# Kernel optimization log

Measured on AMD Instinct MI355X. Metric: run time of the kernel, lower is better.

Reference implementation:

```python
import jax, jax.numpy as jnp
import numpy as np

N, D, K = 40000, 64, 16
E = N * K
EPS = 1e-5  # torch BatchNorm1d default eps


def _bn(h, g, b):
    # BatchNorm1d in training mode: biased batch statistics over dim 0
    m = h.mean(0)
    v = h.var(0)
    return (h - m) * jax.lax.rsqrt(v + EPS) * g + b


def setup_inputs() -> dict:
    key = jax.random.key(0)
    ks = jax.random.split(key, 4)
    kp = jax.random.split(ks[3], 9)

    def w(k, shape):
        return (jax.random.normal(k, shape, dtype=jnp.float32) / np.float32(np.sqrt(shape[0])))

    src = jax.random.randint(ks[2], (E,), 0, N, dtype=jnp.int32)
    dst = jnp.repeat(jnp.arange(N, dtype=jnp.int32), K)  # kNN-style: each node has K in-edges

    return {
        "x": jax.random.normal(ks[0], (N, D), dtype=jnp.float32),
        "pos": jax.random.normal(ks[1], (N, 3), dtype=jnp.float32),
        "edge_index": jnp.stack([src, dst]),
        "W_in": w(kp[0], (D, D)),
        "g1": jnp.ones(D), "b1": jnp.zeros(D),
        "W_v": w(kp[1], (D, D)),
        "W_src": w(kp[2], (D, D)),
        "W_dst": w(kp[3], (D, D)),
        "Wp1": w(kp[4], (3, 3)), "bp1": jnp.zeros(3),
        "gp": jnp.ones(3), "bp": jnp.zeros(3),
        "Wp2": w(kp[5], (3, D)), "bp2": jnp.zeros(D),
        "ga0": jnp.ones(D), "ba0": jnp.zeros(D),
        "Wa1": w(kp[6], (D, D // 8)), "ba1": jnp.zeros(D // 8),
        "ga1": jnp.ones(D // 8), "bb1": jnp.zeros(D // 8),
        "Wa2": w(kp[7], (D // 8, D)), "ba2": jnp.zeros(D),
        "g2": jnp.ones(D), "b2": jnp.zeros(D),
        "W_out": w(kp[8], (D, D)),
        "g3": jnp.ones(D), "b3": jnp.zeros(D),
    }


def reference(x, pos, edge_index, W_in, g1, b1, W_v, W_src, W_dst,
              Wp1, bp1, gp, bp, Wp2, bp2, ga0, ba0, Wa1, ba1, ga1, bb1,
              Wa2, ba2, g2, b2, W_out, g3, b3):
    src, dst = edge_index[0], edge_index[1]  # j (source), i (dest)
    n = x.shape[0]
    x_skip = x
    h = jax.nn.relu(_bn(x @ W_in, g1, b1))

    # PointTransformerConv
    a_src = h @ W_src            # alpha_j projection [N,D]
    a_dst = h @ W_dst            # alpha_i projection [N,D]
    v = h @ W_v                  # value projection  [N,D]
    rel = pos[dst] - pos[src]    # pos_i - pos_j     [E,3]
    ph = jax.nn.relu(_bn(rel @ Wp1 + bp1, gp, bp))
    delta = ph @ Wp2 + bp2       # pos_nn output     [E,D]
    a = a_dst[dst] - a_src[src] + delta
    # attn_nn: BN -> ReLU -> (Lin+BN+ReLU) -> Lin
    a = jax.nn.relu(_bn(a, ga0, ba0))
    a = jax.nn.relu(_bn(a @ Wa1 + ba1, ga1, bb1))
    a = a @ Wa2 + ba2            # [E,D]
    # segment-wise softmax over incoming edges of each dest node
    amax = jax.lax.stop_gradient(jax.ops.segment_max(a, dst, num_segments=n))
    e = jnp.exp(a - amax[dst])
    s = jax.ops.segment_sum(e, dst, num_segments=n)
    attn = e / (s[dst] + 1e-16)  # PyG softmax adds 1e-16
    agg = jax.ops.segment_sum(attn * (v[src] + delta), dst, num_segments=n)

    h = jax.nn.relu(_bn(agg, g2, b2))
    h = _bn(h @ W_out, g3, b3)
    return jax.nn.relu(h + x_skip)
```

## Files before the change

### kernel.cpp

```cpp
#include <hip/hip_runtime.h>

#define NN 40000
#define DDIM 64
#define KE 16
#define EE 640000
#define BNEPS 1e-5f

__device__ __forceinline__ void bn_coeff(const float* __restrict__ S, int C, int c,
                                         const float* __restrict__ g, const float* __restrict__ b,
                                         float inv_n, float& sc, float& sh)
{
    float m   = S[c] * inv_n;
    float var = S[C + c] * inv_n - m * m;
    float r   = rsqrtf(var + BNEPS);
    sc = g[c] * r;
    sh = b[c] - m * sc;
}

template<int TRN>
__global__ __launch_bounds__(256) void gemm64_k(
    const float* __restrict__ in,
    const float* __restrict__ W0, const float* __restrict__ W1, const float* __restrict__ W2,
    float* __restrict__ out0, float* __restrict__ out1, float* __restrict__ out2,
    const float* __restrict__ Sin, const float* __restrict__ gamma, const float* __restrict__ beta,
    float inv_n, float* __restrict__ Sout)
{
    const float* W = (blockIdx.y == 0) ? W0 : ((blockIdx.y == 1) ? W1 : W2);
    float* out     = (blockIdx.y == 0) ? out0 : ((blockIdx.y == 1) ? out1 : out2);

    __shared__ float Wl[64][64];
    __shared__ float inl[64][65];
    __shared__ float scl[64], shl[64];
    __shared__ float ssum[64], ssq[64];

    const int t = threadIdx.x;
    if (t < 64) {
        if (TRN) { float sc, sh; bn_coeff(Sin, 64, t, gamma, beta, inv_n, sc, sh); scl[t] = sc; shl[t] = sh; }
        ssum[t] = 0.f; ssq[t] = 0.f;
    }
#pragma unroll
    for (int i = 0; i < 16; i++) { int idx = t + i * 256; Wl[idx >> 6][idx & 63] = W[idx]; }
    __syncthreads();

    const int rbase = blockIdx.x * 64;
    {
        const int d = t & 63;
        float sc = 0.f, sh = 0.f;
        if (TRN) { sc = scl[d]; sh = shl[d]; }
#pragma unroll
        for (int i = 0; i < 16; i++) {
            int r = (t >> 6) + i * 4;
            float v = in[(size_t)(rbase + r) * 64 + d];
            if (TRN) v = fmaxf(fmaf(v, sc, sh), 0.f);
            inl[r][d] = v;
        }
    }
    __syncthreads();

    const int c0 = (t & 15) * 4, r0 = (t >> 4) * 4;
    float acc[4][4] = {};
#pragma unroll 16
    for (int d = 0; d < 64; d++) {
        float4 w4 = *(const float4*)&Wl[d][c0];
#pragma unroll
        for (int i = 0; i < 4; i++) {
            float h = inl[r0 + i][d];
            acc[i][0] = fmaf(h, w4.x, acc[i][0]);
            acc[i][1] = fmaf(h, w4.y, acc[i][1]);
            acc[i][2] = fmaf(h, w4.z, acc[i][2]);
            acc[i][3] = fmaf(h, w4.w, acc[i][3]);
        }
    }
#pragma unroll
    for (int i = 0; i < 4; i++) {
        float4 o; o.x = acc[i][0]; o.y = acc[i][1]; o.z = acc[i][2]; o.w = acc[i][3];
        *(float4*)&out[(size_t)(rbase + r0 + i) * 64 + c0] = o;
    }
    if (Sout) {
#pragma unroll
        for (int j = 0; j < 4; j++) {
            float s  = acc[0][j] + acc[1][j] + acc[2][j] + acc[3][j];
            float qv = acc[0][j] * acc[0][j] + acc[1][j] * acc[1][j] + acc[2][j] * acc[2][j] + acc[3][j] * acc[3][j];
            atomicAdd(&ssum[c0 + j], s);
            atomicAdd(&ssq[c0 + j], qv);
        }
        __syncthreads();
        if (t < 64) { atomicAdd(&Sout[t], ssum[t]); atomicAdd(&Sout[64 + t], ssq[t]); }
    }
}

__global__ __launch_bounds__(256) void edge_q_k(
    const float* __restrict__ pos, const int* __restrict__ src,
    const float* __restrict__ Wp1, const float* __restrict__ bp1,
    float* __restrict__ q0, float* __restrict__ q1, float* __restrict__ q2,
    float* __restrict__ Sq)
{
    float w00 = Wp1[0], w01 = Wp1[1], w02 = Wp1[2];
    float w10 = Wp1[3], w11 = Wp1[4], w12 = Wp1[5];
    float w20 = Wp1[6], w21 = Wp1[7], w22 = Wp1[8];
    float c0 = bp1[0], c1 = bp1[1], c2 = bp1[2];
    float s0 = 0, s1 = 0, s2 = 0, p0 = 0, p1 = 0, p2 = 0;
    for (int e = blockIdx.x * blockDim.x + threadIdx.x; e < EE; e += gridDim.x * blockDim.x) {
        int sj = src[e]; int di = e >> 4;
        float r0 = pos[di * 3 + 0] - pos[sj * 3 + 0];
        float r1 = pos[di * 3 + 1] - pos[sj * 3 + 1];
        float r2 = pos[di * 3 + 2] - pos[sj * 3 + 2];
        float v0 = c0 + r0 * w00 + r1 * w10 + r2 * w20;
        float v1 = c1 + r0 * w01 + r1 * w11 + r2 * w21;
        float v2 = c2 + r0 * w02 + r1 * w12 + r2 * w22;
        q0[e] = v0; q1[e] = v1; q2[e] = v2;
        s0 += v0; s1 += v1; s2 += v2;
        p0 += v0 * v0; p1 += v1 * v1; p2 += v2 * v2;
    }
#pragma unroll
    for (int o = 32; o > 0; o >>= 1) {
        s0 += __shfl_down(s0, o); s1 += __shfl_down(s1, o); s2 += __shfl_down(s2, o);
        p0 += __shfl_down(p0, o); p1 += __shfl_down(p1, o); p2 += __shfl_down(p2, o);
    }
    __shared__ float sred[4][6];
    const int w = threadIdx.x >> 6;
    if ((threadIdx.x & 63) == 0) {
        sred[w][0] = s0; sred[w][1] = s1; sred[w][2] = s2;
        sred[w][3] = p0; sred[w][4] = p1; sred[w][5] = p2;
    }
    __syncthreads();
    if (threadIdx.x < 6) {
        float v = sred[0][threadIdx.x] + sred[1][threadIdx.x] + sred[2][threadIdx.x] + sred[3][threadIdx.x];
        atomicAdd(&Sq[threadIdx.x], v);
    }
}

__global__ __launch_bounds__(256) void edge_a0_k(
    const float* __restrict__ q0, const float* __restrict__ q1, const float* __restrict__ q2,
    const int* __restrict__ src,
    const float* __restrict__ adst, const float* __restrict__ asrc,
    const float* __restrict__ Wp2, const float* __restrict__ bp2,
    const float* __restrict__ Sq, const float* __restrict__ gp, const float* __restrict__ bp_,
    float* __restrict__ Sa0)
{
    const int lane = threadIdx.x & 63;
    const int r = lane >> 4, fq = lane & 15;
    const int wv   = blockIdx.x * (blockDim.x >> 6) + (threadIdx.x >> 6);
    const int nwv  = gridDim.x * (blockDim.x >> 6);
    const float inv_e = 1.0f / (float)EE;
    float sc30, sh30, sc31, sh31, sc32, sh32;
    bn_coeff(Sq, 3, 0, gp, bp_, inv_e, sc30, sh30);
    bn_coeff(Sq, 3, 1, gp, bp_, inv_e, sc31, sh31);
    bn_coeff(Sq, 3, 2, gp, bp_, inv_e, sc32, sh32);
    float4 w0_4 = *(const float4*)&Wp2[fq * 4];
    float4 w1_4 = *(const float4*)&Wp2[64 + fq * 4];
    float4 w2_4 = *(const float4*)&Wp2[128 + fq * 4];
    float4 bd4  = *(const float4*)&bp2[fq * 4];
    float4 s4 = {0.f,0.f,0.f,0.f}, p4 = {0.f,0.f,0.f,0.f};

    for (int i = wv; i < NN; i += nwv) {
        const int e0 = i << 4;
        float4 ad4 = *(const float4*)&adst[(size_t)i * 64 + fq * 4];
        int   sv  = src[e0 + (lane & 15)];
        float qv0 = q0[e0 + (lane & 15)];
        float qv1 = q1[e0 + (lane & 15)];
        float qv2 = q2[e0 + (lane & 15)];
        int sj[4];
#pragma unroll
        for (int p = 0; p < 4; p++) sj[p] = __shfl(sv, p * 4 + r);
        float4 av[4];
#pragma unroll
        for (int p = 0; p < 4; p++) av[p] = *(const float4*)&asrc[(size_t)sj[p] * 64 + fq * 4];
#pragma unroll
        for (int p = 0; p < 4; p++) {
            int j = p * 4 + r;
            float ph0 = fmaxf(fmaf(__shfl(qv0, j), sc30, sh30), 0.f);
            float ph1 = fmaxf(fmaf(__shfl(qv1, j), sc31, sh31), 0.f);
            float ph2 = fmaxf(fmaf(__shfl(qv2, j), sc32, sh32), 0.f);
            float4 a0v;
            a0v.x = ad4.x - av[p].x + bd4.x + ph0 * w0_4.x + ph1 * w1_4.x + ph2 * w2_4.x;
            a0v.y = ad4.y - av[p].y + bd4.y + ph0 * w0_4.y + ph1 * w1_4.y + ph2 * w2_4.y;
            a0v.z = ad4.z - av[p].z + bd4.z + ph0 * w0_4.z + ph1 * w1_4.z + ph2 * w2_4.z;
            a0v.w = ad4.w - av[p].w + bd4.w + ph0 * w0_4.w + ph1 * w1_4.w + ph2 * w2_4.w;
            s4.x += a0v.x; s4.y += a0v.y; s4.z += a0v.z; s4.w += a0v.w;
            p4.x = fmaf(a0v.x, a0v.x, p4.x); p4.y = fmaf(a0v.y, a0v.y, p4.y);
            p4.z = fmaf(a0v.z, a0v.z, p4.z); p4.w = fmaf(a0v.w, a0v.w, p4.w);
        }
    }
    s4.x += __shfl_xor(s4.x, 16); s4.y += __shfl_xor(s4.y, 16);
    s4.z += __shfl_xor(s4.z, 16); s4.w += __shfl_xor(s4.w, 16);
    p4.x += __shfl_xor(p4.x, 16); p4.y += __shfl_xor(p4.y, 16);
    p4.z += __shfl_xor(p4.z, 16); p4.w += __shfl_xor(p4.w, 16);
    s4.x += __shfl_xor(s4.x, 32); s4.y += __shfl_xor(s4.y, 32);
    s4.z += __shfl_xor(s4.z, 32); s4.w += __shfl_xor(s4.w, 32);
    p4.x += __shfl_xor(p4.x, 32); p4.y += __shfl_xor(p4.y, 32);
    p4.z += __shfl_xor(p4.z, 32); p4.w += __shfl_xor(p4.w, 32);

    __shared__ float ls[64], lq[64];
    if (threadIdx.x < 64) { ls[threadIdx.x] = 0.f; lq[threadIdx.x] = 0.f; }
    __syncthreads();
    if (lane < 16) {
        atomicAdd(&ls[fq * 4 + 0], s4.x); atomicAdd(&ls[fq * 4 + 1], s4.y);
        atomicAdd(&ls[fq * 4 + 2], s4.z); atomicAdd(&ls[fq * 4 + 3], s4.w);
        atomicAdd(&lq[fq * 4 + 0], p4.x); atomicAdd(&lq[fq * 4 + 1], p4.y);
        atomicAdd(&lq[fq * 4 + 2], p4.z); atomicAdd(&lq[fq * 4 + 3], p4.w);
    }
    __syncthreads();
    if (threadIdx.x < 64) { atomicAdd(&Sa0[threadIdx.x], ls[threadIdx.x]); atomicAdd(&Sa0[64 + threadIdx.x], lq[threadIdx.x]); }
}

__global__ __launch_bounds__(256) void edge_t_k(
    const float* __restrict__ q0, const float* __restrict__ q1, const float* __restrict__ q2,
    const int* __restrict__ src,
    const float* __restrict__ adst, const float* __restrict__ asrc,
    const float* __restrict__ Wp2, const float* __restrict__ bp2,
    const float* __restrict__ Sq, const float* __restrict__ gp, const float* __restrict__ bp_,
    const float* __restrict__ Sa0, const float* __restrict__ ga0, const float* __restrict__ ba0,
    const float* __restrict__ Wa1, const float* __restrict__ ba1,
    float* __restrict__ tout, float* __restrict__ St)
{
    __shared__ float a1l[64][68];
    __shared__ float wl[64][8];
    __shared__ float red[16];
    const int t = threadIdx.x;
    const int lane = t & 63;
    const int w = t >> 6;
    const int r = lane >> 4, fq = lane & 15;
    const float inv_e = 1.0f / (float)EE;
    float sc30, sh30, sc31, sh31, sc32, sh32;
    bn_coeff(Sq, 3, 0, gp, bp_, inv_e, sc30, sh30);
    bn_coeff(Sq, 3, 1, gp, bp_, inv_e, sc31, sh31);
    bn_coeff(Sq, 3, 2, gp, bp_, inv_e, sc32, sh32);
    float4 scA4, shA4;
    bn_coeff(Sa0, 64, fq * 4 + 0, ga0, ba0, inv_e, scA4.x, shA4.x);
    bn_coeff(Sa0, 64, fq * 4 + 1, ga0, ba0, inv_e, scA4.y, shA4.y);
    bn_coeff(Sa0, 64, fq * 4 + 2, ga0, ba0, inv_e, scA4.z, shA4.z);
    bn_coeff(Sa0, 64, fq * 4 + 3, ga0, ba0, inv_e, scA4.w, shA4.w);
    float4 w0_4 = *(const float4*)&Wp2[fq * 4];
    float4 w1_4 = *(const float4*)&Wp2[64 + fq * 4];
    float4 w2_4 = *(const float4*)&Wp2[128 + fq * 4];
    float4 bd4  = *(const float4*)&bp2[fq * 4];
    for (int i = t; i < 512; i += 256) wl[i >> 3][i & 7] = Wa1[i];
    if (t < 16) red[t] = 0.f;

    const int eL = t >> 2;
    const int j0 = (t & 3) * 2;
    float bA = ba1[j0], bB = ba1[j0 + 1];
    float ssA = 0.f, spA = 0.f, ssB = 0.f, spB = 0.f;

    for (int g = blockIdx.x; g < NN / 4; g += gridDim.x) {
        __syncthreads();
        {
            const int i  = g * 4 + w;
            const int e0 = i << 4;
            float4 ad4 = *(const float4*)&adst[(size_t)i * 64 + fq * 4];
            int   sv  = src[e0 + (lane & 15)];
            float qv0 = q0[e0 + (lane & 15)];
            float qv1 = q1[e0 + (lane & 15)];
            float qv2 = q2[e0 + (lane & 15)];
            int sj[4];
#pragma unroll
            for (int p = 0; p < 4; p++) sj[p] = __shfl(sv, p * 4 + r);
            float4 av[4];
#pragma unroll
            for (int p = 0; p < 4; p++) av[p] = *(const float4*)&asrc[(size_t)sj[p] * 64 + fq * 4];
#pragma unroll
            for (int p = 0; p < 4; p++) {
                int j = p * 4 + r;
                float ph0 = fmaxf(fmaf(__shfl(qv0, j), sc30, sh30), 0.f);
                float ph1 = fmaxf(fmaf(__shfl(qv1, j), sc31, sh31), 0.f);
                float ph2 = fmaxf(fmaf(__shfl(qv2, j), sc32, sh32), 0.f);
                float4 a1v;
                a1v.x = ad4.x - av[p].x + bd4.x + ph0 * w0_4.x + ph1 * w1_4.x + ph2 * w2_4.x;
                a1v.y = ad4.y - av[p].y + bd4.y + ph0 * w0_4.y + ph1 * w1_4.y + ph2 * w2_4.y;
                a1v.z = ad4.z - av[p].z + bd4.z + ph0 * w0_4.z + ph1 * w1_4.z + ph2 * w2_4.z;
                a1v.w = ad4.w - av[p].w + bd4.w + ph0 * w0_4.w + ph1 * w1_4.w + ph2 * w2_4.w;
                a1v.x = fmaxf(fmaf(a1v.x, scA4.x, shA4.x), 0.f);
                a1v.y = fmaxf(fmaf(a1v.y, scA4.y, shA4.y), 0.f);
                a1v.z = fmaxf(fmaf(a1v.z, scA4.z, shA4.z), 0.f);
                a1v.w = fmaxf(fmaf(a1v.w, scA4.w, shA4.w), 0.f);
                *(float4*)&a1l[w * 16 + j][fq * 4] = a1v;
            }
        }
        __syncthreads();
        {
            float acc0 = bA, acc1 = bB;
#pragma unroll 16
            for (int dd = 0; dd < 64; dd++) {
                float a = a1l[eL][dd];
                acc0 = fmaf(a, wl[dd][j0], acc0);
                acc1 = fmaf(a, wl[dd][j0 + 1], acc1);
            }
            int e = g * 64 + eL;
            float2 o; o.x = acc0; o.y = acc1;
            *(float2*)&tout[(size_t)e * 8 + j0] = o;
            ssA += acc0; spA += acc0 * acc0;
            ssB += acc1; spB += acc1 * acc1;
        }
    }
    __syncthreads();
    atomicAdd(&red[j0], ssA);     atomicAdd(&red[j0 + 1], ssB);
    atomicAdd(&red[8 + j0], spA); atomicAdd(&red[8 + j0 + 1], spB);
    __syncthreads();
    if (t < 16) atomicAdd(&St[t], red[t]);
}

__global__ __launch_bounds__(256) void edge_final_k(
    const float* __restrict__ tin,
    const float* __restrict__ q0, const float* __restrict__ q1, const float* __restrict__ q2,
    const int* __restrict__ src, const float* __restrict__ vv,
    const float* __restrict__ Wp2, const float* __restrict__ bp2,
    const float* __restrict__ Sq, const float* __restrict__ gp, const float* __restrict__ bp_,
    const float* __restrict__ St, const float* __restrict__ ga1, const float* __restrict__ bb1,
    const float* __restrict__ Wa2, const float* __restrict__ ba2,
    float* __restrict__ agg, float* __restrict__ Sagg)
{
    __shared__ float att_l[4][16][68];
    __shared__ float tt_l[4][16][8];
    __shared__ float ls[64], lq[64];
    const int t = threadIdx.x, lane = t & 63, w = t >> 6;
    const int r = lane >> 4, fq = lane & 15;
    const float inv_e = 1.0f / (float)EE;
    float sc3[3], sh3[3];
#pragma unroll
    for (int k = 0; k < 3; k++) bn_coeff(Sq, 3, k, gp, bp_, inv_e, sc3[k], sh3[k]);
    float sc8[8], sh8[8];
#pragma unroll
    for (int k = 0; k < 8; k++) bn_coeff(St, 8, k, ga1, bb1, inv_e, sc8[k], sh8[k]);
    float wa[8];
#pragma unroll
    for (int k = 0; k < 8; k++) wa[k] = Wa2[k * 64 + lane];
    float bad = ba2[lane];
    float4 wp0_4 = *(const float4*)&Wp2[fq * 4];
    float4 wp1_4 = *(const float4*)&Wp2[64 + fq * 4];
    float4 wp2_4 = *(const float4*)&Wp2[128 + fq * 4];
    float4 bpd4  = *(const float4*)&bp2[fq * 4];
    float4 ssum4 = {0.f, 0.f, 0.f, 0.f}, ssq4 = {0.f, 0.f, 0.f, 0.f};

    for (int nn = 0; nn < 4; nn++) {
        const int i  = blockIdx.x * 16 + nn * 4 + w;
        const int e0 = i << 4;
        if (lane < 32) {
            float4 v = *(const float4*)&tin[(size_t)e0 * 8 + lane * 4];
            ((float4*)&tt_l[w][0][0])[lane] = v;
        }
        int   sv  = src[e0 + (lane & 15)];
        float qv0 = q0[e0 + (lane & 15)];
        float qv1 = q1[e0 + (lane & 15)];
        float qv2 = q2[e0 + (lane & 15)];
        __syncthreads();
        {
            float ax[16];
            float m = -3.0e38f;
#pragma unroll
            for (int j = 0; j < 16; j++) {
                float4 ta = *(const float4*)&tt_l[w][j][0];
                float4 tb = *(const float4*)&tt_l[w][j][4];
                float a = bad;
                a = fmaf(fmaxf(fmaf(ta.x, sc8[0], sh8[0]), 0.f), wa[0], a);
                a = fmaf(fmaxf(fmaf(ta.y, sc8[1], sh8[1]), 0.f), wa[1], a);
                a = fmaf(fmaxf(fmaf(ta.z, sc8[2], sh8[2]), 0.f), wa[2], a);
                a = fmaf(fmaxf(fmaf(ta.w, sc8[3], sh8[3]), 0.f), wa[3], a);
                a = fmaf(fmaxf(fmaf(tb.x, sc8[4], sh8[4]), 0.f), wa[4], a);
                a = fmaf(fmaxf(fmaf(tb.y, sc8[5], sh8[5]), 0.f), wa[5], a);
                a = fmaf(fmaxf(fmaf(tb.z, sc8[6], sh8[6]), 0.f), wa[6], a);
                a = fmaf(fmaxf(fmaf(tb.w, sc8[7], sh8[7]), 0.f), wa[7], a);
                ax[j] = a; m = fmaxf(m, a);
            }
            float s = 0.f;
#pragma unroll
            for (int j = 0; j < 16; j++) { ax[j] = __expf(ax[j] - m); s += ax[j]; }
            float inv = 1.0f / (s + 1e-16f);
#pragma unroll
            for (int j = 0; j < 16; j++) att_l[w][j][lane] = ax[j] * inv;
        }
        __syncthreads();
        {
            float4 acc = {0.f, 0.f, 0.f, 0.f};
#pragma unroll
            for (int p = 0; p < 4; p++) {
                int j  = p * 4 + r;
                int sj = __shfl(sv, j);
                float4 v4  = *(const float4*)&vv[(size_t)sj * 64 + fq * 4];
                float4 at4 = *(const float4*)&att_l[w][j][fq * 4];
                float ph0 = fmaxf(fmaf(__shfl(qv0, j), sc3[0], sh3[0]), 0.f);
                float ph1 = fmaxf(fmaf(__shfl(qv1, j), sc3[1], sh3[1]), 0.f);
                float ph2 = fmaxf(fmaf(__shfl(qv2, j), sc3[2], sh3[2]), 0.f);
                float4 dl4;
                dl4.x = bpd4.x + ph0 * wp0_4.x + ph1 * wp1_4.x + ph2 * wp2_4.x;
                dl4.y = bpd4.y + ph0 * wp0_4.y + ph1 * wp1_4.y + ph2 * wp2_4.y;
                dl4.z = bpd4.z + ph0 * wp0_4.z + ph1 * wp1_4.z + ph2 * wp2_4.z;
                dl4.w = bpd4.w + ph0 * wp0_4.w + ph1 * wp1_4.w + ph2 * wp2_4.w;
                acc.x = fmaf(at4.x, v4.x + dl4.x, acc.x);
                acc.y = fmaf(at4.y, v4.y + dl4.y, acc.y);
                acc.z = fmaf(at4.z, v4.z + dl4.z, acc.z);
                acc.w = fmaf(at4.w, v4.w + dl4.w, acc.w);
            }
            acc.x += __shfl_xor(acc.x, 16); acc.y += __shfl_xor(acc.y, 16);
            acc.z += __shfl_xor(acc.z, 16); acc.w += __shfl_xor(acc.w, 16);
            acc.x += __shfl_xor(acc.x, 32); acc.y += __shfl_xor(acc.y, 32);
            acc.z += __shfl_xor(acc.z, 32); acc.w += __shfl_xor(acc.w, 32);
            if (lane < 16) {
                *(float4*)&agg[(size_t)i * 64 + lane * 4] = acc;
                ssum4.x += acc.x; ssum4.y += acc.y; ssum4.z += acc.z; ssum4.w += acc.w;
                ssq4.x  += acc.x * acc.x; ssq4.y += acc.y * acc.y;
                ssq4.z  += acc.z * acc.z; ssq4.w += acc.w * acc.w;
            }
        }
        __syncthreads();
    }
    if (t < 64) { ls[t] = 0.f; lq[t] = 0.f; }
    __syncthreads();
    if (lane < 16) {
        atomicAdd(&ls[fq * 4 + 0], ssum4.x); atomicAdd(&ls[fq * 4 + 1], ssum4.y);
        atomicAdd(&ls[fq * 4 + 2], ssum4.z); atomicAdd(&ls[fq * 4 + 3], ssum4.w);
        atomicAdd(&lq[fq * 4 + 0], ssq4.x);  atomicAdd(&lq[fq * 4 + 1], ssq4.y);
        atomicAdd(&lq[fq * 4 + 2], ssq4.z);  atomicAdd(&lq[fq * 4 + 3], ssq4.w);
    }
    __syncthreads();
    if (t < 64) { atomicAdd(&Sagg[t], ls[t]); atomicAdd(&Sagg[64 + t], lq[t]); }
}

__global__ __launch_bounds__(256) void final_k(
    const float* __restrict__ t2, const float* __restrict__ x,
    const float* __restrict__ St2, const float* __restrict__ g3, const float* __restrict__ b3,
    float* __restrict__ out)
{
    __shared__ float scl[64], shl[64];
    const int t = threadIdx.x;
    if (t < 64) { float sc, sh; bn_coeff(St2, 64, t, g3, b3, 1.0f / (float)NN, sc, sh); scl[t] = sc; shl[t] = sh; }
    __syncthreads();
    int idx = blockIdx.x * 256 + t;
    int c0 = (idx & 15) * 4;
    const float4 a = *(const float4*)&t2[(size_t)idx * 4];
    const float4 b = *(const float4*)&x[(size_t)idx * 4];
    float4 o;
    o.x = fmaxf(fmaf(a.x, scl[c0 + 0], shl[c0 + 0]) + b.x, 0.f);
    o.y = fmaxf(fmaf(a.y, scl[c0 + 1], shl[c0 + 1]) + b.y, 0.f);
    o.z = fmaxf(fmaf(a.z, scl[c0 + 2], shl[c0 + 2]) + b.z, 0.f);
    o.w = fmaxf(fmaf(a.w, scl[c0 + 3], shl[c0 + 3]) + b.w, 0.f);
    *(float4*)&out[(size_t)idx * 4] = o;
}

extern "C" void kernel_launch(void* const* d_in, const int* in_sizes, int n_in,
                              void* d_out, int out_size, void* d_ws, size_t ws_size,
                              hipStream_t stream)
{
    const float* x    = (const float*)d_in[0];
    const float* pos  = (const float*)d_in[1];
    const int*   src  = (const int*)d_in[2];
    const float* W_in = (const float*)d_in[3];
    const float* g1   = (const float*)d_in[4];
    const float* b1   = (const float*)d_in[5];
    const float* W_v  = (const float*)d_in[6];
    const float* W_src= (const float*)d_in[7];
    const float* W_dst= (const float*)d_in[8];
    const float* Wp1  = (const float*)d_in[9];
    const float* bp1  = (const float*)d_in[10];
    const float* gp   = (const float*)d_in[11];
    const float* bp_  = (const float*)d_in[12];
    const float* Wp2  = (const float*)d_in[13];
    const float* bp2  = (const float*)d_in[14];
    const float* ga0  = (const float*)d_in[15];
    const float* ba0  = (const float*)d_in[16];
    const float* Wa1  = (const float*)d_in[17];
    const float* ba1  = (const float*)d_in[18];
    const float* ga1  = (const float*)d_in[19];
    const float* bb1  = (const float*)d_in[20];
    const float* Wa2  = (const float*)d_in[21];
    const float* ba2  = (const float*)d_in[22];
    const float* g2   = (const float*)d_in[23];
    const float* b2   = (const float*)d_in[24];
    const float* W_out= (const float*)d_in[25];
    const float* g3   = (const float*)d_in[26];
    const float* b3   = (const float*)d_in[27];
    float* out = (float*)d_out;

    float* wsf   = (float*)d_ws;
    float* S_t1  = wsf;
    float* S_q   = wsf + 128;
    float* S_a0  = wsf + 192;
    float* S_t   = wsf + 320;
    float* S_agg = wsf + 384;
    float* S_t2  = wsf + 512;
    const size_t N64 = (size_t)NN * 64;
    float* t1   = wsf + 1024;
    float* asrc = t1 + N64;
    float* adst = asrc + N64;
    float* vv   = adst + N64;
    float* q0   = vv + N64;
    float* q1   = q0 + EE;
    float* q2   = q1 + EE;
    float* tt   = q2 + EE;
    float* agg  = t1;
    float* t2   = asrc;

    hipMemsetAsync(wsf, 0, 1024 * sizeof(float), stream);

    gemm64_k<0><<<dim3(625, 1), 256, 0, stream>>>(x, W_in, W_in, W_in, t1, t1, t1,
                                                  nullptr, nullptr, nullptr, 0.f, S_t1);
    gemm64_k<1><<<dim3(625, 3), 256, 0, stream>>>(t1, W_src, W_dst, W_v, asrc, adst, vv,
                                                  S_t1, g1, b1, 1.0f / (float)NN, nullptr);
    edge_q_k<<<256, 256, 0, stream>>>(pos, src, Wp1, bp1, q0, q1, q2, S_q);
    edge_a0_k<<<2048, 256, 0, stream>>>(q0, q1, q2, src, adst, asrc, Wp2, bp2, S_q, gp, bp_, S_a0);
    edge_t_k<<<2048, 256, 0, stream>>>(q0, q1, q2, src, adst, asrc, Wp2, bp2, S_q, gp, bp_,
                                       S_a0, ga0, ba0, Wa1, ba1, tt, S_t);
    edge_final_k<<<2500, 256, 0, stream>>>(tt, q0, q1, q2, src, vv, Wp2, bp2, S_q, gp, bp_,
                                           S_t, ga1, bb1, Wa2, ba2, agg, S_agg);
    gemm64_k<1><<<dim3(625, 1), 256, 0, stream>>>(agg, W_out, W_out, W_out, t2, t2, t2,
                                                  S_agg, g2, b2, 1.0f / (float)NN, S_t2);
    final_k<<<2500, 256, 0, stream>>>(t2, x, S_t2, g3, b3, out);
}
```

Before: 292.7 us.

## Pack per-edge q and src into float4; compute Wa1 projection in registers with shuffles

Per-edge position features q0/q1/q2 and the source index are now stored together as one float4 per edge. The three edge kernels fetch them with a single vector load instead of four scalar loads. edge_t_k drops its shared-memory staging of the activations and its two block barriers per group. Each lane now multiplies its 4 features by a register-held slice of Wa1 and the 8 outputs are summed across 16 lanes with xor shuffles. This adds many shuffles and more register use per edge in exchange for less shared-memory traffic and synchronisation.

```diff
diff --git a/kernel.cpp b/kernel.cpp
--- a/kernel.cpp
+++ b/kernel.cpp
@@ -92,8 +92,7 @@
 __global__ __launch_bounds__(256) void edge_q_k(
     const float* __restrict__ pos, const int* __restrict__ src,
     const float* __restrict__ Wp1, const float* __restrict__ bp1,
-    float* __restrict__ q0, float* __restrict__ q1, float* __restrict__ q2,
-    float* __restrict__ Sq)
+    float4* __restrict__ q4, float* __restrict__ Sq)
 {
     float w00 = Wp1[0], w01 = Wp1[1], w02 = Wp1[2];
     float w10 = Wp1[3], w11 = Wp1[4], w12 = Wp1[5];
@@ -108,7 +107,8 @@
         float v0 = c0 + r0 * w00 + r1 * w10 + r2 * w20;
         float v1 = c1 + r0 * w01 + r1 * w11 + r2 * w21;
         float v2 = c2 + r0 * w02 + r1 * w12 + r2 * w22;
-        q0[e] = v0; q1[e] = v1; q2[e] = v2;
+        float4 o; o.x = v0; o.y = v1; o.z = v2; o.w = __int_as_float(sj);
+        q4[e] = o;
         s0 += v0; s1 += v1; s2 += v2;
         p0 += v0 * v0; p1 += v1 * v1; p2 += v2 * v2;
     }
@@ -131,8 +131,7 @@
 }
 
 __global__ __launch_bounds__(256) void edge_a0_k(
-    const float* __restrict__ q0, const float* __restrict__ q1, const float* __restrict__ q2,
-    const int* __restrict__ src,
+    const float4* __restrict__ q4v,
     const float* __restrict__ adst, const float* __restrict__ asrc,
     const float* __restrict__ Wp2, const float* __restrict__ bp2,
     const float* __restrict__ Sq, const float* __restrict__ gp, const float* __restrict__ bp_,
@@ -156,10 +155,8 @@
     for (int i = wv; i < NN; i += nwv) {
         const int e0 = i << 4;
         float4 ad4 = *(const float4*)&adst[(size_t)i * 64 + fq * 4];
-        int   sv  = src[e0 + (lane & 15)];
-        float qv0 = q0[e0 + (lane & 15)];
-        float qv1 = q1[e0 + (lane & 15)];
-        float qv2 = q2[e0 + (lane & 15)];
+        float4 qs  = q4v[e0 + (lane & 15)];
+        int sv = __float_as_int(qs.w);
         int sj[4];
 #pragma unroll
         for (int p = 0; p < 4; p++) sj[p] = __shfl(sv, p * 4 + r);
@@ -169,9 +166,9 @@
 #pragma unroll
         for (int p = 0; p < 4; p++) {
             int j = p * 4 + r;
-            float ph0 = fmaxf(fmaf(__shfl(qv0, j), sc30, sh30), 0.f);
-            float ph1 = fmaxf(fmaf(__shfl(qv1, j), sc31, sh31), 0.f);
-            float ph2 = fmaxf(fmaf(__shfl(qv2, j), sc32, sh32), 0.f);
+            float ph0 = fmaxf(fmaf(__shfl(qs.x, j), sc30, sh30), 0.f);
+            float ph1 = fmaxf(fmaf(__shfl(qs.y, j), sc31, sh31), 0.f);
+            float ph2 = fmaxf(fmaf(__shfl(qs.z, j), sc32, sh32), 0.f);
             float4 a0v;
             a0v.x = ad4.x - av[p].x + bd4.x + ph0 * w0_4.x + ph1 * w1_4.x + ph2 * w2_4.x;
             a0v.y = ad4.y - av[p].y + bd4.y + ph0 * w0_4.y + ph1 * w1_4.y + ph2 * w2_4.y;
@@ -205,8 +202,7 @@
 }
 
 __global__ __launch_bounds__(256) void edge_t_k(
-    const float* __restrict__ q0, const float* __restrict__ q1, const float* __restrict__ q2,
-    const int* __restrict__ src,
+    const float4* __restrict__ q4v,
     const float* __restrict__ adst, const float* __restrict__ asrc,
     const float* __restrict__ Wp2, const float* __restrict__ bp2,
     const float* __restrict__ Sq, const float* __restrict__ gp, const float* __restrict__ bp_,
@@ -214,13 +210,12 @@
     const float* __restrict__ Wa1, const float* __restrict__ ba1,
     float* __restrict__ tout, float* __restrict__ St)
 {
-    __shared__ float a1l[64][68];
-    __shared__ float wl[64][8];
+    __shared__ float t_l[4][16][8];
     __shared__ float red[16];
-    const int t = threadIdx.x;
-    const int lane = t & 63;
-    const int w = t >> 6;
+    const int t = threadIdx.x, lane = t & 63, w = t >> 6;
     const int r = lane >> 4, fq = lane & 15;
+    const int wv  = blockIdx.x * 4 + w;
+    const int nwv = gridDim.x * 4;
     const float inv_e = 1.0f / (float)EE;
     float sc30, sh30, sc31, sh31, sc32, sh32;
     bn_coeff(Sq, 3, 0, gp, bp_, inv_e, sc30, sh30);
@@ -235,75 +230,92 @@
     float4 w1_4 = *(const float4*)&Wp2[64 + fq * 4];
     float4 w2_4 = *(const float4*)&Wp2[128 + fq * 4];
     float4 bd4  = *(const float4*)&bp2[fq * 4];
-    for (int i = t; i < 512; i += 256) wl[i >> 3][i & 7] = Wa1[i];
+    float wAf[4][8];
+#pragma unroll
+    for (int d = 0; d < 4; d++) {
+        float4 lo = *(const float4*)&Wa1[(size_t)(fq * 4 + d) * 8];
+        float4 hi = *(const float4*)&Wa1[(size_t)(fq * 4 + d) * 8 + 4];
+        wAf[d][0] = lo.x; wAf[d][1] = lo.y; wAf[d][2] = lo.z; wAf[d][3] = lo.w;
+        wAf[d][4] = hi.x; wAf[d][5] = hi.y; wAf[d][6] = hi.z; wAf[d][7] = hi.w;
+    }
+    float bb[8];
+    {
+        float4 lo = *(const float4*)&ba1[0];
+        float4 hi = *(const float4*)&ba1[4];
+        bb[0] = lo.x; bb[1] = lo.y; bb[2] = lo.z; bb[3] = lo.w;
+        bb[4] = hi.x; bb[5] = hi.y; bb[6] = hi.z; bb[7] = hi.w;
+    }
+    float ss[8] = {}, sp[8] = {};
     if (t < 16) red[t] = 0.f;
-
-    const int eL = t >> 2;
-    const int j0 = (t & 3) * 2;
-    float bA = ba1[j0], bB = ba1[j0 + 1];
-    float ssA = 0.f, spA = 0.f, ssB = 0.f, spB = 0.f;
-
-    for (int g = blockIdx.x; g < NN / 4; g += gridDim.x) {
-        __syncthreads();
-        {
-            const int i  = g * 4 + w;
-            const int e0 = i << 4;
-            float4 ad4 = *(const float4*)&adst[(size_t)i * 64 + fq * 4];
-            int   sv  = src[e0 + (lane & 15)];
-            float qv0 = q0[e0 + (lane & 15)];
-            float qv1 = q1[e0 + (lane & 15)];
-            float qv2 = q2[e0 + (lane & 15)];
-            int sj[4];
-#pragma unroll
-            for (int p = 0; p < 4; p++) sj[p] = __shfl(sv, p * 4 + r);
-            float4 av[4];
-#pragma unroll
-            for (int p = 0; p < 4; p++) av[p] = *(const float4*)&asrc[(size_t)sj[p] * 64 + fq * 4];
-#pragma unroll
-            for (int p = 0; p < 4; p++) {
-                int j = p * 4 + r;
-                float ph0 = fmaxf(fmaf(__shfl(qv0, j), sc30, sh30), 0.f);
-                float ph1 = fmaxf(fmaf(__shfl(qv1, j), sc31, sh31), 0.f);
-                float ph2 = fmaxf(fmaf(__shfl(qv2, j), sc32, sh32), 0.f);
-                float4 a1v;
-                a1v.x = ad4.x - av[p].x + bd4.x + ph0 * w0_4.x + ph1 * w1_4.x + ph2 * w2_4.x;
-                a1v.y = ad4.y - av[p].y + bd4.y + ph0 * w0_4.y + ph1 * w1_4.y + ph2 * w2_4.y;
-                a1v.z = ad4.z - av[p].z + bd4.z + ph0 * w0_4.z + ph1 * w1_4.z + ph2 * w2_4.z;
-                a1v.w = ad4.w - av[p].w + bd4.w + ph0 * w0_4.w + ph1 * w1_4.w + ph2 * w2_4.w;
-                a1v.x = fmaxf(fmaf(a1v.x, scA4.x, shA4.x), 0.f);
-                a1v.y = fmaxf(fmaf(a1v.y, scA4.y, shA4.y), 0.f);
-                a1v.z = fmaxf(fmaf(a1v.z, scA4.z, shA4.z), 0.f);
-                a1v.w = fmaxf(fmaf(a1v.w, scA4.w, shA4.w), 0.f);
-                *(float4*)&a1l[w * 16 + j][fq * 4] = a1v;
+    __syncthreads();
+
+    for (int i = wv; i < NN; i += nwv) {
+        const int e0 = i << 4;
+        float4 ad4 = *(const float4*)&adst[(size_t)i * 64 + fq * 4];
+        float4 qs  = q4v[e0 + (lane & 15)];
+        int sv = __float_as_int(qs.w);
+        int sj[4];
+#pragma unroll
+        for (int p = 0; p < 4; p++) sj[p] = __shfl(sv, p * 4 + r);
+        float4 av[4];
+#pragma unroll
+        for (int p = 0; p < 4; p++) av[p] = *(const float4*)&asrc[(size_t)sj[p] * 64 + fq * 4];
+#pragma unroll
+        for (int p = 0; p < 4; p++) {
+            int j = p * 4 + r;
+            float ph0 = fmaxf(fmaf(__shfl(qs.x, j), sc30, sh30), 0.f);
+            float ph1 = fmaxf(fmaf(__shfl(qs.y, j), sc31, sh31), 0.f);
+            float ph2 = fmaxf(fmaf(__shfl(qs.z, j), sc32, sh32), 0.f);
+            float4 a1v;
+            a1v.x = ad4.x - av[p].x + bd4.x + ph0 * w0_4.x + ph1 * w1_4.x + ph2 * w2_4.x;
+            a1v.y = ad4.y - av[p].y + bd4.y + ph0 * w0_4.y + ph1 * w1_4.y + ph2 * w2_4.y;
+            a1v.z = ad4.z - av[p].z + bd4.z + ph0 * w0_4.z + ph1 * w1_4.z + ph2 * w2_4.z;
+            a1v.w = ad4.w - av[p].w + bd4.w + ph0 * w0_4.w + ph1 * w1_4.w + ph2 * w2_4.w;
+            a1v.x = fmaxf(fmaf(a1v.x, scA4.x, shA4.x), 0.f);
+            a1v.y = fmaxf(fmaf(a1v.y, scA4.y, shA4.y), 0.f);
+            a1v.z = fmaxf(fmaf(a1v.z, scA4.z, shA4.z), 0.f);
+            a1v.w = fmaxf(fmaf(a1v.w, scA4.w, shA4.w), 0.f);
+            float part[8];
+#pragma unroll
+            for (int k = 0; k < 8; k++) {
+                part[k] = a1v.x * wAf[0][k] + a1v.y * wAf[1][k]
+                        + a1v.z * wAf[2][k] + a1v.w * wAf[3][k];
             }
-        }
-        __syncthreads();
-        {
-            float acc0 = bA, acc1 = bB;
-#pragma unroll 16
-            for (int dd = 0; dd < 64; dd++) {
-                float a = a1l[eL][dd];
-                acc0 = fmaf(a, wl[dd][j0], acc0);
-                acc1 = fmaf(a, wl[dd][j0 + 1], acc1);
+#pragma unroll
+            for (int k = 0; k < 8; k++) {
+                part[k] += __shfl_xor(part[k], 1);
+                part[k] += __shfl_xor(part[k], 2);
+                part[k] += __shfl_xor(part[k], 4);
+                part[k] += __shfl_xor(part[k], 8);
             }
-            int e = g * 64 + eL;
-            float2 o; o.x = acc0; o.y = acc1;
-            *(float2*)&tout[(size_t)e * 8 + j0] = o;
-            ssA += acc0; spA += acc0 * acc0;
-            ssB += acc1; spB += acc1 * acc1;
-        }
-    }
-    __syncthreads();
-    atomicAdd(&red[j0], ssA);     atomicAdd(&red[j0 + 1], ssB);
-    atomicAdd(&red[8 + j0], spA); atomicAdd(&red[8 + j0 + 1], spB);
+            if (fq == 0) {
+#pragma unroll
+                for (int k = 0; k < 8; k++) {
+                    float v = part[k] + bb[k];
+                    t_l[w][p * 4 + r][k] = v;
+                    ss[k] += v; sp[k] = fmaf(v, v, sp[k]);
+                }
+            }
+        }
+        float2 o = *(const float2*)&t_l[w][lane >> 2][(lane & 3) * 2];
+        *(float2*)&tout[(size_t)e0 * 8 + lane * 2] = o;
+    }
+#pragma unroll
+    for (int k = 0; k < 8; k++) {
+        ss[k] += __shfl_xor(ss[k], 16); ss[k] += __shfl_xor(ss[k], 32);
+        sp[k] += __shfl_xor(sp[k], 16); sp[k] += __shfl_xor(sp[k], 32);
+    }
+    if (lane == 0) {
+#pragma unroll
+        for (int k = 0; k < 8; k++) { atomicAdd(&red[k], ss[k]); atomicAdd(&red[8 + k], sp[k]); }
+    }
     __syncthreads();
     if (t < 16) atomicAdd(&St[t], red[t]);
 }
 
 __global__ __launch_bounds__(256) void edge_final_k(
     const float* __restrict__ tin,
-    const float* __restrict__ q0, const float* __restrict__ q1, const float* __restrict__ q2,
-    const int* __restrict__ src, const float* __restrict__ vv,
+    const float4* __restrict__ q4v, const float* __restrict__ vv,
     const float* __restrict__ Wp2, const float* __restrict__ bp2,
     const float* __restrict__ Sq, const float* __restrict__ gp, const float* __restrict__ bp_,
     const float* __restrict__ St, const float* __restrict__ ga1, const float* __restrict__ bb1,
@@ -339,10 +351,8 @@
             float4 v = *(const float4*)&tin[(size_t)e0 * 8 + lane * 4];
             ((float4*)&tt_l[w][0][0])[lane] = v;
         }
-        int   sv  = src[e0 + (lane & 15)];
-        float qv0 = q0[e0 + (lane & 15)];
-        float qv1 = q1[e0 + (lane & 15)];
-        float qv2 = q2[e0 + (lane & 15)];
+        float4 qs = q4v[e0 + (lane & 15)];
+        int sv = __float_as_int(qs.w);
         __syncthreads();
         {
             float ax[16];
@@ -378,9 +388,9 @@
                 int sj = __shfl(sv, j);
                 float4 v4  = *(const float4*)&vv[(size_t)sj * 64 + fq * 4];
                 float4 at4 = *(const float4*)&att_l[w][j][fq * 4];
-                float ph0 = fmaxf(fmaf(__shfl(qv0, j), sc3[0], sh3[0]), 0.f);
-                float ph1 = fmaxf(fmaf(__shfl(qv1, j), sc3[1], sh3[1]), 0.f);
-                float ph2 = fmaxf(fmaf(__shfl(qv2, j), sc3[2], sh3[2]), 0.f);
+                float ph0 = fmaxf(fmaf(__shfl(qs.x, j), sc3[0], sh3[0]), 0.f);
+                float ph1 = fmaxf(fmaf(__shfl(qs.y, j), sc3[1], sh3[1]), 0.f);
+                float ph2 = fmaxf(fmaf(__shfl(qs.z, j), sc3[2], sh3[2]), 0.f);
                 float4 dl4;
                 dl4.x = bpd4.x + ph0 * wp0_4.x + ph1 * wp1_4.x + ph2 * wp2_4.x;
                 dl4.y = bpd4.y + ph0 * wp0_4.y + ph1 * wp1_4.y + ph2 * wp2_4.y;
@@ -483,10 +493,8 @@
     float* asrc = t1 + N64;
     float* adst = asrc + N64;
     float* vv   = adst + N64;
-    float* q0   = vv + N64;
-    float* q1   = q0 + EE;
-    float* q2   = q1 + EE;
-    float* tt   = q2 + EE;
+    float* q4   = vv + N64;
+    float* tt   = q4 + 4 * (size_t)EE;
     float* agg  = t1;
     float* t2   = asrc;
 
@@ -496,11 +504,11 @@
                                                   nullptr, nullptr, nullptr, 0.f, S_t1);
     gemm64_k<1><<<dim3(625, 3), 256, 0, stream>>>(t1, W_src, W_dst, W_v, asrc, adst, vv,
                                                   S_t1, g1, b1, 1.0f / (float)NN, nullptr);
-    edge_q_k<<<256, 256, 0, stream>>>(pos, src, Wp1, bp1, q0, q1, q2, S_q);
-    edge_a0_k<<<2048, 256, 0, stream>>>(q0, q1, q2, src, adst, asrc, Wp2, bp2, S_q, gp, bp_, S_a0);
-    edge_t_k<<<2048, 256, 0, stream>>>(q0, q1, q2, src, adst, asrc, Wp2, bp2, S_q, gp, bp_,
+    edge_q_k<<<256, 256, 0, stream>>>(pos, src, Wp1, bp1, (float4*)q4, S_q);
+    edge_a0_k<<<2048, 256, 0, stream>>>((const float4*)q4, adst, asrc, Wp2, bp2, S_q, gp, bp_, S_a0);
+    edge_t_k<<<2048, 256, 0, stream>>>((const float4*)q4, adst, asrc, Wp2, bp2, S_q, gp, bp_,
                                        S_a0, ga0, ba0, Wa1, ba1, tt, S_t);
-    edge_final_k<<<2500, 256, 0, stream>>>(tt, q0, q1, q2, src, vv, Wp2, bp2, S_q, gp, bp_,
+    edge_final_k<<<2500, 256, 0, stream>>>(tt, (const float4*)q4, vv, Wp2, bp2, S_q, gp, bp_,
                                            S_t, ga1, bb1, Wa2, ba2, agg, S_agg);
     gemm64_k<1><<<dim3(625, 1), 256, 0, stream>>>(agg, W_out, W_out, W_out, t2, t2, t2,
                                                   S_agg, g2, b2, 1.0f / (float)NN, S_t2);
```

After: 322.4 us. 10.2% more time.
